# Performance work log

Hardware: AMD Instinct MI355X
Metric: run time of the kernel (lower is better)

Reference implementation:

```python
import jax, jax.numpy as jnp
import numpy as np
import math

WINDOW_LEFT = 512   # sliding-window: each query attends to keys in [q-512, q]
WINDOW_RIGHT = 0    # causal
NEG_INF = -1e30


def setup_inputs() -> dict:
    key = jax.random.key(0)
    kq, kk, kv, ks = jax.random.split(key, 4)
    B, S, H, D = 2, 2048, 16, 128
    q = jax.random.normal(kq, (B, S, H, D), dtype=jnp.float32)
    k = jax.random.normal(kk, (B, S, H, D), dtype=jnp.float32)
    v = jax.random.normal(kv, (B, S, H, D), dtype=jnp.float32)
    # geometric-ish ALiBi slopes per head (positive, decaying), like flash-attn
    alibi_slopes = jax.random.uniform(ks, (H,), dtype=jnp.float32, minval=0.001, maxval=0.5)
    return {"q": q, "k": k, "v": v, "alibi_slopes": alibi_slopes}


def reference(q, k, v, alibi_slopes):
    # q,k,v: [B, S, H, D]; alibi_slopes: [H]
    B, S, H, D = q.shape
    scale = 1.0 / math.sqrt(D)
    # scores: [B, H, Sq, Sk]
    scores = jnp.einsum("bqhd,bkhd->bhqk", q, k) * scale
    qi = jnp.arange(S)[:, None]
    ki = jnp.arange(S)[None, :]
    rel = ki - qi  # [Sq, Sk], <=0 for past keys
    # ALiBi bias (equal q/k lengths): -slope * |q - k|
    alibi = -alibi_slopes[:, None, None] * jnp.abs(rel).astype(scores.dtype)  # [H,Sq,Sk]
    scores = scores + alibi[None, :, :, :]
    # causal + sliding-window mask: allow WINDOW_RIGHT future, WINDOW_LEFT past
    mask = (rel <= WINDOW_RIGHT) & (rel >= -WINDOW_LEFT)  # [Sq, Sk]
    scores = jnp.where(mask[None, None, :, :], scores, NEG_INF)
    p = jax.nn.softmax(scores, axis=-1)
    out = jnp.einsum("bhqk,bkhd->bqhd", p, v)
    return out
```

## Files before the change

### kernel.cpp

```cpp
#include <hip/hip_runtime.h>
#include <hip/hip_bf16.h>

typedef __attribute__((ext_vector_type(8))) __bf16 bf16x8;
typedef __attribute__((ext_vector_type(2))) __bf16 bf16x2;
typedef __attribute__((ext_vector_type(4))) float f32x4;

#define MFMA32(a, b, c) __builtin_amdgcn_mfma_f32_16x16x32_bf16((a), (b), (c), 0, 0, 0)

constexpr int Bc = 2, Sc = 2048, Hc = 16, Dc = 128;
constexpr int HD = Hc * Dc;
constexpr int QB = 128;
constexpr float SCALE = 0.0883883476483184405f;
constexpr float NEGF = -30000.0f;
constexpr int KSTR = 2080;

__device__ inline bf16x8 cvt8(f32x4 a, f32x4 b) {
    bf16x8 r;
    r[0]=(__bf16)a[0]; r[1]=(__bf16)a[1]; r[2]=(__bf16)a[2]; r[3]=(__bf16)a[3];
    r[4]=(__bf16)b[0]; r[5]=(__bf16)b[1]; r[6]=(__bf16)b[2]; r[7]=(__bf16)b[3];
    return r;
}

__global__ __launch_bounds__(512, 4) void lumen_attn_kernel(
    const float* __restrict__ Q, const float* __restrict__ K,
    const float* __restrict__ V, const float* __restrict__ SLP,
    float* __restrict__ O)
{
    __shared__ __align__(16) char k_lds[64 * 256];
    __shared__ __align__(16) char v_lds[8 * KSTR];
    __shared__ __align__(16) char p_lds[8][16 * 128];

    const int tid  = threadIdx.x;
    const int lane = tid & 63;
    const int wid  = tid >> 6;
    const int cl = lane & 15;
    const int kg = lane >> 4;
    const int r0 = kg << 2;

    const int bid = blockIdx.x;
    const int swz = (bid & 7) * 64 + (bid >> 3);
    const int qb  = (swz & 15) * QB;
    const int bh  = swz >> 4;
    const int h = bh & 15, b = bh >> 4;

    const float slope = SLP[h];
    const size_t base = (size_t)b * Sc * HD + (size_t)h * Dc;
    const float* qp = Q + base;
    const float* kp = K + base;
    const float* vp = V + base;
    float*       op = O + base;

    const int qw = qb + wid * 16;

    bf16x8 qf[4];
    {
        const float* qrow = qp + (size_t)(qw + cl) * HD + kg * 8;
        #pragma unroll
        for (int c = 0; c < 4; ++c) {
            f32x4 a = *(const f32x4*)(qrow + c * 32);
            f32x4 bq = *(const f32x4*)(qrow + c * 32 + 4);
            #pragma unroll
            for (int i = 0; i < 4; ++i) { a[i] *= SCALE; bq[i] *= SCALE; }
            qf[c] = cvt8(a, bq);
        }
    }

    f32x4 o_acc[8];
    #pragma unroll
    for (int nn = 0; nn < 8; ++nn) o_acc[nn] = f32x4{0.f, 0.f, 0.f, 0.f};
    f32x4 ssum = f32x4{0.f, 0.f, 0.f, 0.f};

    bf16x8 ones8;
    #pragma unroll
    for (int i = 0; i < 8; ++i) ones8[i] = (__bf16)1.0f;

    int voff[8];
    #pragma unroll
    for (int nn = 0; nn < 8; ++nn) {
        const int d = nn * 16 + cl;
        const int s = (d & ~7) | ((d & 7) ^ ((d >> 3) & 7));
        voff[nn] = s * 16;
    }

    const int kb0    = qb > 512 ? qb - 512 : 0;
    const int kb_end = qb + QB - 64;

    const int tk = tid >> 4;
    const int td = (tid & 15) * 8;
    const int a_ = tid & 15;
    const int ksw = (tk & 7) << 4;

    char* const pw = p_lds[wid];

    for (int kb = kb0; kb <= kb_end; kb += 64) {
        __syncthreads();

        #pragma unroll
        for (int p = 0; p < 2; ++p) {
            const int k = p * 32 + tk;
            const float* kr = kp + (size_t)(kb + k) * HD + td;
            bf16x8 k8 = cvt8(*(const f32x4*)kr, *(const f32x4*)(kr + 4));
            *(bf16x8*)(k_lds + k * 256 + ((td * 2) ^ ksw)) = k8;
        }
        {
            const float* v0_ = vp + (size_t)(kb + 2 * tk) * HD + td;
            const float* v1_ = vp + (size_t)(kb + 2 * tk + 1) * HD + td;
            bf16x8 vA8 = cvt8(*(const f32x4*)v0_, *(const f32x4*)(v0_ + 4));
            bf16x8 vB8 = cvt8(*(const f32x4*)v1_, *(const f32x4*)(v1_ + 4));
            char* vdst = v_lds + (tk >> 2) * KSTR + (tk & 3) * 4;
            #pragma unroll
            for (int j = 0; j < 8; ++j) {
                const int s = a_ * 8 + (j ^ (a_ & 7));
                bf16x2 pk;
                pk[0] = vA8[j]; pk[1] = vB8[j];
                *(bf16x2*)(vdst + s * 16) = pk;
            }
        }
        __syncthreads();

        if (kb > qw + 15 || kb + 63 < qw - 512) continue;

        f32x4 sacc[4];
        #pragma unroll
        for (int n = 0; n < 4; ++n) sacc[n] = f32x4{0.f, 0.f, 0.f, 0.f};
        #pragma unroll
        for (int n = 0; n < 4; ++n) {
            const int key = n * 16 + cl;
            const char* kbse = k_lds + key * 256;
            const int sw = (key & 7) << 4;
            #pragma unroll
            for (int c = 0; c < 4; ++c) {
                bf16x8 kf = *(const bf16x8*)(kbse + ((kg * 16 + c * 64) ^ sw));
                sacc[n] = MFMA32(qf[c], kf, sacc[n]);
            }
        }

        const int relc = (qw + r0) - (kb + cl);
        #pragma unroll
        for (int j = 0; j < 4; ++j) {
            char* prw = pw + (r0 + j) * 128;
            const int swp = ((r0 + j) & 7) << 4;
            #pragma unroll
            for (int n = 0; n < 4; ++n) {
                const int rel = relc + (j - 16 * n);
                const float bias = ((unsigned)rel <= 512u) ? (-slope * (float)rel) : NEGF;
                const float pe = __expf(sacc[n][j] + bias);
                *(__bf16*)(prw + (((n * 16 + cl) * 2) ^ swp)) = (__bf16)pe;
            }
        }

        asm volatile("s_waitcnt lgkmcnt(0)" ::: "memory");

        const int psw = (cl & 7) << 4;
        #pragma unroll
        for (int kk = 0; kk < 2; ++kk) {
            bf16x8 pa = *(const bf16x8*)(pw + cl * 128 + ((kk * 64 + kg * 16) ^ psw));
            ssum = MFMA32(pa, ones8, ssum);
            const char* vko = v_lds + (kk * 4 + kg) * KSTR;
            #pragma unroll
            for (int nn = 0; nn < 8; ++nn) {
                bf16x8 vf = *(const bf16x8*)(vko + voff[nn]);
                o_acc[nn] = MFMA32(pa, vf, o_acc[nn]);
            }
        }
    }

    #pragma unroll
    for (int j = 0; j < 4; ++j) {
        float inv = 1.0f / ssum[j];
        float* orow = op + (size_t)(qw + r0 + j) * HD;
        #pragma unroll
        for (int nn = 0; nn < 8; ++nn)
            orow[nn * 16 + cl] = o_acc[nn][j] * inv;
    }
}

extern "C" void kernel_launch(void* const* d_in, const int* in_sizes, int n_in,
                              void* d_out, int out_size, void* d_ws, size_t ws_size,
                              hipStream_t stream) {
    const float* q   = (const float*)d_in[0];
    const float* k   = (const float*)d_in[1];
    const float* v   = (const float*)d_in[2];
    const float* slp = (const float*)d_in[3];
    float* out = (float*)d_out;

    dim3 grid(Bc * Hc * (Sc / QB));
    lumen_attn_kernel<<<grid, dim3(512), 0, stream>>>(q, k, v, slp, out);
}
```

Measured before the change: 57.36 us.

## Give each wave 32 query rows, halve block size, compute row sums on scalar

```diff
diff --git a/kernel.cpp b/kernel.cpp
--- a/kernel.cpp
+++ b/kernel.cpp
@@ -2,6 +2,7 @@
 #include <hip/hip_bf16.h>
 
 typedef __attribute__((ext_vector_type(8))) __bf16 bf16x8;
+typedef __attribute__((ext_vector_type(4))) __bf16 bf16x4;
 typedef __attribute__((ext_vector_type(2))) __bf16 bf16x2;
 typedef __attribute__((ext_vector_type(4))) float f32x4;
 
@@ -21,14 +22,14 @@
     return r;
 }
 
-__global__ __launch_bounds__(512, 4) void lumen_attn_kernel(
+__global__ __launch_bounds__(256, 3) void lumen_attn_kernel(
     const float* __restrict__ Q, const float* __restrict__ K,
     const float* __restrict__ V, const float* __restrict__ SLP,
     float* __restrict__ O)
 {
     __shared__ __align__(16) char k_lds[64 * 256];
     __shared__ __align__(16) char v_lds[8 * KSTR];
-    __shared__ __align__(16) char p_lds[8][16 * 128];
+    __shared__ __align__(16) char p_lds[4][32 * 128];
 
     const int tid  = threadIdx.x;
     const int lane = tid & 63;
@@ -50,29 +51,28 @@
     const float* vp = V + base;
     float*       op = O + base;
 
-    const int qw = qb + wid * 16;
-
-    bf16x8 qf[4];
-    {
-        const float* qrow = qp + (size_t)(qw + cl) * HD + kg * 8;
+    const int qw = qb + wid * 32;
+
+    bf16x8 qf[2][4];
+    #pragma unroll
+    for (int s = 0; s < 2; ++s) {
+        const float* qrow = qp + (size_t)(qw + s * 16 + cl) * HD + kg * 8;
         #pragma unroll
         for (int c = 0; c < 4; ++c) {
             f32x4 a = *(const f32x4*)(qrow + c * 32);
             f32x4 bq = *(const f32x4*)(qrow + c * 32 + 4);
             #pragma unroll
             for (int i = 0; i < 4; ++i) { a[i] *= SCALE; bq[i] *= SCALE; }
-            qf[c] = cvt8(a, bq);
-        }
-    }
-
-    f32x4 o_acc[8];
-    #pragma unroll
-    for (int nn = 0; nn < 8; ++nn) o_acc[nn] = f32x4{0.f, 0.f, 0.f, 0.f};
-    f32x4 ssum = f32x4{0.f, 0.f, 0.f, 0.f};
-
-    bf16x8 ones8;
-    #pragma unroll
-    for (int i = 0; i < 8; ++i) ones8[i] = (__bf16)1.0f;
+            qf[s][c] = cvt8(a, bq);
+        }
+    }
+
+    f32x4 o_acc[2][8];
+    #pragma unroll
+    for (int s = 0; s < 2; ++s)
+        #pragma unroll
+        for (int nn = 0; nn < 8; ++nn) o_acc[s][nn] = f32x4{0.f, 0.f, 0.f, 0.f};
+    float ssum[2] = {0.f, 0.f};
 
     int voff[8];
     #pragma unroll
@@ -85,10 +85,9 @@
     const int kb0    = qb > 512 ? qb - 512 : 0;
     const int kb_end = qb + QB - 64;
 
-    const int tk = tid >> 4;
-    const int td = (tid & 15) * 8;
-    const int a_ = tid & 15;
-    const int ksw = (tk & 7) << 4;
+    const int tk5 = tid >> 3;
+    const int t8  = tid & 7;
+    const int d0  = t8 * 16;
 
     char* const pw = p_lds[wid];
 
@@ -97,81 +96,114 @@
 
         #pragma unroll
         for (int p = 0; p < 2; ++p) {
-            const int k = p * 32 + tk;
-            const float* kr = kp + (size_t)(kb + k) * HD + td;
-            bf16x8 k8 = cvt8(*(const f32x4*)kr, *(const f32x4*)(kr + 4));
-            *(bf16x8*)(k_lds + k * 256 + ((td * 2) ^ ksw)) = k8;
+            const int k = p * 32 + tk5;
+            const float* kr = kp + (size_t)(kb + k) * HD + d0;
+            bf16x8 kA = cvt8(*(const f32x4*)kr,       *(const f32x4*)(kr + 4));
+            bf16x8 kB = cvt8(*(const f32x4*)(kr + 8), *(const f32x4*)(kr + 12));
+            char* kbse = k_lds + k * 256;
+            const int sw = (k & 15) << 4;
+            *(bf16x8*)(kbse + ((d0 * 2) ^ sw))      = kA;
+            *(bf16x8*)(kbse + ((d0 * 2 + 16) ^ sw)) = kB;
         }
         {
-            const float* v0_ = vp + (size_t)(kb + 2 * tk) * HD + td;
-            const float* v1_ = vp + (size_t)(kb + 2 * tk + 1) * HD + td;
-            bf16x8 vA8 = cvt8(*(const f32x4*)v0_, *(const f32x4*)(v0_ + 4));
-            bf16x8 vB8 = cvt8(*(const f32x4*)v1_, *(const f32x4*)(v1_ + 4));
-            char* vdst = v_lds + (tk >> 2) * KSTR + (tk & 3) * 4;
+            const float* v0_ = vp + (size_t)(kb + 2 * tk5) * HD + d0;
+            const float* v1_ = v0_ + HD;
+            bf16x8 vA0 = cvt8(*(const f32x4*)v0_,       *(const f32x4*)(v0_ + 4));
+            bf16x8 vA1 = cvt8(*(const f32x4*)(v0_ + 8), *(const f32x4*)(v0_ + 12));
+            bf16x8 vB0 = cvt8(*(const f32x4*)v1_,       *(const f32x4*)(v1_ + 4));
+            bf16x8 vB1 = cvt8(*(const f32x4*)(v1_ + 8), *(const f32x4*)(v1_ + 12));
+            char* vdst = v_lds + (tk5 >> 2) * KSTR + (tk5 & 3) * 4;
             #pragma unroll
             for (int j = 0; j < 8; ++j) {
-                const int s = a_ * 8 + (j ^ (a_ & 7));
-                bf16x2 pk;
-                pk[0] = vA8[j]; pk[1] = vB8[j];
+                const int d = d0 + j;
+                const int s = (d & ~7) | ((d & 7) ^ ((d >> 3) & 7));
+                bf16x2 pk; pk[0] = vA0[j]; pk[1] = vB0[j];
                 *(bf16x2*)(vdst + s * 16) = pk;
             }
+            #pragma unroll
+            for (int j = 0; j < 8; ++j) {
+                const int d = d0 + 8 + j;
+                const int s = (d & ~7) | ((d & 7) ^ ((d >> 3) & 7));
+                bf16x2 pk; pk[0] = vA1[j]; pk[1] = vB1[j];
+                *(bf16x2*)(vdst + s * 16) = pk;
+            }
         }
         __syncthreads();
 
-        if (kb > qw + 15 || kb + 63 < qw - 512) continue;
-
-        f32x4 sacc[4];
-        #pragma unroll
-        for (int n = 0; n < 4; ++n) sacc[n] = f32x4{0.f, 0.f, 0.f, 0.f};
+        if (kb > qw + 31 || kb + 63 < qw - 512) continue;
+
+        f32x4 sacc[2][4];
+        #pragma unroll
+        for (int s = 0; s < 2; ++s)
+            #pragma unroll
+            for (int n = 0; n < 4; ++n) sacc[s][n] = f32x4{0.f, 0.f, 0.f, 0.f};
         #pragma unroll
         for (int n = 0; n < 4; ++n) {
-            const int key = n * 16 + cl;
-            const char* kbse = k_lds + key * 256;
-            const int sw = (key & 7) << 4;
+            const char* kbse = k_lds + (n * 16 + cl) * 256;
+            const int sw = cl << 4;
             #pragma unroll
             for (int c = 0; c < 4; ++c) {
-                bf16x8 kf = *(const bf16x8*)(kbse + ((kg * 16 + c * 64) ^ sw));
-                sacc[n] = MFMA32(qf[c], kf, sacc[n]);
-            }
-        }
-
-        const int relc = (qw + r0) - (kb + cl);
-        #pragma unroll
-        for (int j = 0; j < 4; ++j) {
-            char* prw = pw + (r0 + j) * 128;
-            const int swp = ((r0 + j) & 7) << 4;
+                bf16x8 kf = *(const bf16x8*)(kbse + (((c * 32 + kg * 8) * 2) ^ sw));
+                sacc[0][n] = MFMA32(kf, qf[0][c], sacc[0][n]);
+                sacc[1][n] = MFMA32(kf, qf[1][c], sacc[1][n]);
+            }
+        }
+
+        #pragma unroll
+        for (int s = 0; s < 2; ++s) {
+            const int q = qw + s * 16 + cl;
+            char* prow = pw + (s * 16 + cl) * 128;
+            const int swp = (cl & 7) << 4;
             #pragma unroll
             for (int n = 0; n < 4; ++n) {
-                const int rel = relc + (j - 16 * n);
-                const float bias = ((unsigned)rel <= 512u) ? (-slope * (float)rel) : NEGF;
-                const float pe = __expf(sacc[n][j] + bias);
-                *(__bf16*)(prw + (((n * 16 + cl) * 2) ^ swp)) = (__bf16)pe;
+                bf16x4 pk;
+                #pragma unroll
+                for (int j = 0; j < 4; ++j) {
+                    const int key = kb + n * 16 + r0 + j;
+                    const int rel = q - key;
+                    const float val = ((unsigned)rel <= 512u)
+                                      ? fmaf(-slope, (float)rel, sacc[s][n][j]) : NEGF;
+                    const float pe = __expf(val);
+                    ssum[s] += pe;
+                    pk[j] = (__bf16)pe;
+                }
+                *(bf16x4*)(prow + (((n * 16 + r0) * 2) ^ swp)) = pk;
             }
         }
 
         asm volatile("s_waitcnt lgkmcnt(0)" ::: "memory");
 
-        const int psw = (cl & 7) << 4;
         #pragma unroll
         for (int kk = 0; kk < 2; ++kk) {
-            bf16x8 pa = *(const bf16x8*)(pw + cl * 128 + ((kk * 64 + kg * 16) ^ psw));
-            ssum = MFMA32(pa, ones8, ssum);
+            const int off = ((kk * 32 + kg * 8) * 2) ^ ((cl & 7) << 4);
+            bf16x8 pa0 = *(const bf16x8*)(pw + cl * 128 + off);
+            bf16x8 pa1 = *(const bf16x8*)(pw + (16 + cl) * 128 + off);
             const char* vko = v_lds + (kk * 4 + kg) * KSTR;
             #pragma unroll
             for (int nn = 0; nn < 8; ++nn) {
                 bf16x8 vf = *(const bf16x8*)(vko + voff[nn]);
-                o_acc[nn] = MFMA32(pa, vf, o_acc[nn]);
-            }
-        }
-    }
-
-    #pragma unroll
-    for (int j = 0; j < 4; ++j) {
-        float inv = 1.0f / ssum[j];
-        float* orow = op + (size_t)(qw + r0 + j) * HD;
-        #pragma unroll
-        for (int nn = 0; nn < 8; ++nn)
-            orow[nn * 16 + cl] = o_acc[nn][j] * inv;
+                o_acc[0][nn] = MFMA32(pa0, vf, o_acc[0][nn]);
+                o_acc[1][nn] = MFMA32(pa1, vf, o_acc[1][nn]);
+            }
+        }
+    }
+
+    #pragma unroll
+    for (int s = 0; s < 2; ++s) {
+        ssum[s] += __shfl_xor(ssum[s], 16);
+        ssum[s] += __shfl_xor(ssum[s], 32);
+    }
+    #pragma unroll
+    for (int s = 0; s < 2; ++s) {
+        #pragma unroll
+        for (int j = 0; j < 4; ++j) {
+            const float sj = __shfl(ssum[s], r0 + j);
+            const float inv = 1.0f / sj;
+            float* orow = op + (size_t)(qw + s * 16 + r0 + j) * HD;
+            #pragma unroll
+            for (int nn = 0; nn < 8; ++nn)
+                orow[nn * 16 + cl] = o_acc[s][nn][j] * inv;
+        }
     }
 }
 
@@ -185,5 +217,5 @@
     float* out = (float*)d_out;
 
     dim3 grid(Bc * Hc * (Sc / QB));
-    lumen_attn_kernel<<<grid, dim3(512), 0, stream>>>(q, k, v, slp, out);
+    lumen_attn_kernel<<<grid, dim3(256), 0, stream>>>(q, k, v, slp, out);
 }
```

Result: slower. 92.82 us (+61.8%).
